# Performance work log

Hardware: AMD Instinct MI355X
Metric: run time of the kernel (lower is better)

The kernel has to match this reference:

```python
import jax, jax.numpy as jnp
import numpy as np

N_HEAD = 16
LN_EPS = 1e-5
NEG = -10000.0


def layer_norm(x, g, b):
    mu = jnp.mean(x, axis=-1, keepdims=True)
    var = jnp.mean((x - mu) ** 2, axis=-1, keepdims=True)
    return (x - mu) * jax.lax.rsqrt(var + LN_EPS) * g + b


def split_heads(t):
    B, S, D = t.shape
    return t.reshape(B, S, N_HEAD, D // N_HEAD).transpose(0, 2, 1, 3)  # [B,H,S,hd]


def merge_heads(t):
    B, H, S, hd = t.shape
    return t.transpose(0, 2, 1, 3).reshape(B, S, H * hd)


def attn_core(q, k, v, causal):
    hd = v.shape[-1]
    w = jnp.einsum('bhqd,bhkd->bhqk', q, k) / jnp.sqrt(jnp.float32(hd)).astype(q.dtype)
    if causal:
        S = w.shape[-1]
        mask = jnp.tril(jnp.ones((S, S), dtype=bool))
        w = jnp.where(mask[None, None], w, jnp.asarray(NEG, w.dtype))
    w = jax.nn.softmax(w, axis=-1)
    return jnp.einsum('bhqk,bhkd->bhqd', w, v)


def setup_inputs() -> dict:
    key = jax.random.key(0)
    ks = jax.random.split(key, 12)
    B, S, D = 4, 1024, 1024
    sd = 0.02
    inp = {
        'x': jax.random.normal(ks[0], (B, S, D), jnp.float32),
        'ctx': jax.random.normal(ks[1], (B, S, D), jnp.float32),
        'c_attn_w': jax.random.normal(ks[2], (D, 3 * D), jnp.float32) * sd,
        'c_attn_b': jnp.zeros((3 * D,), jnp.float32),
        'self_proj_w': jax.random.normal(ks[3], (D, D), jnp.float32) * sd,
        'self_proj_b': jnp.zeros((D,), jnp.float32),
        'q_w': jax.random.normal(ks[4], (D, D), jnp.float32) * sd,
        'q_b': jnp.zeros((D,), jnp.float32),
        'kv_w': jax.random.normal(ks[5], (D, 2 * D), jnp.float32) * sd,
        'kv_b': jnp.zeros((2 * D,), jnp.float32),
        'cross_proj_w': jax.random.normal(ks[6], (D, D), jnp.float32) * sd,
        'cross_proj_b': jnp.zeros((D,), jnp.float32),
        'fc_w': jax.random.normal(ks[7], (D, 4 * D), jnp.float32) * sd,
        'fc_b': jnp.zeros((4 * D,), jnp.float32),
        'mlp_proj_w': jax.random.normal(ks[8], (4 * D, D), jnp.float32) * sd,
        'mlp_proj_b': jnp.zeros((D,), jnp.float32),
        'ln1_g': jnp.ones((D,), jnp.float32), 'ln1_b': jnp.zeros((D,), jnp.float32),
        'ln2_g': jnp.ones((D,), jnp.float32), 'ln2_b': jnp.zeros((D,), jnp.float32),
        'ln3_g': jnp.ones((D,), jnp.float32), 'ln3_b': jnp.zeros((D,), jnp.float32),
    }
    return inp


def reference(x, ctx, c_attn_w, c_attn_b, self_proj_w, self_proj_b,
              q_w, q_b, kv_w, kv_b, cross_proj_w, cross_proj_b,
              fc_w, fc_b, mlp_proj_w, mlp_proj_b,
              ln1_g, ln1_b, ln2_g, ln2_b, ln3_g, ln3_b):
    D = x.shape[-1]
    # --- causal self-attention (post-LN residual) ---
    qkv = x @ c_attn_w + c_attn_b
    q, k, v = jnp.split(qkv, 3, axis=-1)
    a = attn_core(split_heads(q), split_heads(k), split_heads(v), causal=True)
    a = merge_heads(a) @ self_proj_w + self_proj_b
    x = layer_norm(x + a, ln1_g, ln1_b)
    # --- cross-attention ---
    q = x @ q_w + q_b
    kv = ctx @ kv_w + kv_b
    k, v = jnp.split(kv, 2, axis=-1)
    a = attn_core(split_heads(q), split_heads(k), split_heads(v), causal=False)
    a = merge_heads(a) @ cross_proj_w + cross_proj_b
    x = layer_norm(x + a, ln2_g, ln2_b)
    # --- MLP (GPT2 gelu_new == tanh-approx gelu) ---
    h = jax.nn.gelu(x @ fc_w + fc_b, approximate=True)
    m = h @ mlp_proj_w + mlp_proj_b
    x = layer_norm(x + m, ln3_g, ln3_b)
    return x
```

## Files before the change

kernel.cpp:

```cpp
#include <hip/hip_runtime.h>

typedef unsigned short u16;
typedef unsigned int   u32;
typedef short bf16x8 __attribute__((ext_vector_type(8)));
typedef unsigned short u16x8 __attribute__((ext_vector_type(8)));
typedef float f32x4 __attribute__((ext_vector_type(4)));

__device__ __forceinline__ float bf2f(u16 u) {
    u32 x = ((u32)u) << 16;
    return __builtin_bit_cast(float, x);
}
__device__ __forceinline__ u16 f2bf(float f) {
    u32 u = __builtin_bit_cast(u32, f);
    u += 0x7fffu + ((u >> 16) & 1u);
    return (u16)(u >> 16);
}
__device__ __forceinline__ float gelu_f(float x) {
    const float u = 0.7978845608028654f * (x + 0.044715f * x * x * x);
    const float e = __expf(-2.f * fabsf(u));
    const float t = __builtin_copysignf((1.f - e) / (1.f + e), u);
    return 0.5f * x * (1.f + t);
}
__device__ __forceinline__ void glds16(const u16* g, u16* l) {
    __builtin_amdgcn_global_load_lds((const __attribute__((address_space(1))) u32*)g,
                                     (__attribute__((address_space(3))) u32*)l, 16, 0, 0);
}

__global__ void sniff_kernel(const u32* __restrict__ p, int* __restrict__ flag) {
    const int i = threadIdx.x;
    const u32 w = p[i * 8191 + 5];
    const u32 e = (w >> 7) & 0xFF;
    const bool absurd = (e >= 1 && e <= 90) || (e >= 160 && e <= 254);
    const unsigned long long m = __ballot(absurd);
    if (i == 0) *flag = (__popcll(m) >= 8) ? 1 : 0;
}

struct CvtPack {
    const void* src[15];
    u16*        dst[15];
    int         n[15];
};
__global__ __launch_bounds__(256) void cvt_many(CvtPack pp, const int* __restrict__ flag) {
    const int f = *flag;
    const int j = blockIdx.y;
    const void* src = pp.src[j];
    u16* dst = pp.dst[j];
    const int n = pp.n[j];
    const int idx = blockIdx.x * 256 + threadIdx.x;
    const int stride = gridDim.x * 256;
    if (f) {
        const float* s = (const float*)src;
        for (int i = idx; i < n; i += stride) dst[i] = f2bf(s[i]);
    } else {
        const u16* s = (const u16*)src;
        for (int i = idx; i < n; i += stride) dst[i] = s[i];
    }
}

__global__ __launch_bounds__(256) void transpose_cv(const void* __restrict__ src,
                                                    u16* __restrict__ dst,
                                                    int Kd, int Nd,
                                                    const int* __restrict__ flag) {
    const int f = *flag;
    __shared__ u16 t[32][33];
    const int tx = threadIdx.x & 31, ty = threadIdx.x >> 5;
    const int x  = blockIdx.x * 32 + tx;
    const int y0 = blockIdx.y * 32;
#pragma unroll
    for (int j = 0; j < 4; ++j) {
        const long idx = (long)(y0 + ty + j * 8) * Nd + x;
        t[ty + j * 8][tx] = f ? f2bf(((const float*)src)[idx]) : ((const u16*)src)[idx];
    }
    __syncthreads();
    const int xo = blockIdx.y * 32 + tx;
#pragma unroll
    for (int j = 0; j < 4; ++j)
        dst[(long)(blockIdx.x * 32 + ty + j * 8) * Kd + xo] = t[tx][ty + j * 8];
}

__global__ __launch_bounds__(256) void ln_kernel(u16* __restrict__ x,
                                                 const u16* __restrict__ g,
                                                 const u16* __restrict__ bta) {
    const int tid = threadIdx.x;
    u16* p = x + (long)blockIdx.x * 1024;
    float v[4];
    float s = 0.f, s2 = 0.f;
#pragma unroll
    for (int i = 0; i < 4; ++i) {
        v[i] = bf2f(p[tid + i * 256]);
        s += v[i]; s2 += v[i] * v[i];
    }
#pragma unroll
    for (int off = 32; off; off >>= 1) {
        s  += __shfl_xor(s, off, 64);
        s2 += __shfl_xor(s2, off, 64);
    }
    __shared__ float ps[8];
    if ((tid & 63) == 0) { ps[(tid >> 6) * 2] = s; ps[(tid >> 6) * 2 + 1] = s2; }
    __syncthreads();
    s  = ps[0] + ps[2] + ps[4] + ps[6];
    s2 = ps[1] + ps[3] + ps[5] + ps[7];
    const float mu  = s * (1.f / 1024.f);
    const float var = s2 * (1.f / 1024.f) - mu * mu;
    const float rs  = rsqrtf(var + 1e-5f);
#pragma unroll
    for (int i = 0; i < 4; ++i) {
        const int c = tid + i * 256;
        p[c] = f2bf((v[i] - mu) * rs * bf2f(g[c]) + bf2f(bta[c]));
    }
}

__global__ __launch_bounds__(256) void ln_out_kernel(const u16* __restrict__ xin,
                                                     const u16* __restrict__ g,
                                                     const u16* __restrict__ bta,
                                                     void* __restrict__ out,
                                                     const int* __restrict__ flag) {
    const int tid = threadIdx.x;
    const u16* p = xin + (long)blockIdx.x * 1024;
    float v[4];
    float s = 0.f, s2 = 0.f;
#pragma unroll
    for (int i = 0; i < 4; ++i) {
        v[i] = bf2f(p[tid + i * 256]);
        s += v[i]; s2 += v[i] * v[i];
    }
#pragma unroll
    for (int off = 32; off; off >>= 1) {
        s  += __shfl_xor(s, off, 64);
        s2 += __shfl_xor(s2, off, 64);
    }
    __shared__ float ps[8];
    if ((tid & 63) == 0) { ps[(tid >> 6) * 2] = s; ps[(tid >> 6) * 2 + 1] = s2; }
    __syncthreads();
    s  = ps[0] + ps[2] + ps[4] + ps[6];
    s2 = ps[1] + ps[3] + ps[5] + ps[7];
    const float mu  = s * (1.f / 1024.f);
    const float var = s2 * (1.f / 1024.f) - mu * mu;
    const float rs  = rsqrtf(var + 1e-5f);
    const int f = *flag;
    if (f) {
        float* o = (float*)out + (long)blockIdx.x * 1024;
#pragma unroll
        for (int i = 0; i < 4; ++i) {
            const int c = tid + i * 256;
            o[c] = (v[i] - mu) * rs * bf2f(g[c]) + bf2f(bta[c]);
        }
    } else {
        u16* o = (u16*)out + (long)blockIdx.x * 1024;
#pragma unroll
        for (int i = 0; i < 4; ++i) {
            const int c = tid + i * 256;
            o[c] = f2bf((v[i] - mu) * rs * bf2f(g[c]) + bf2f(bta[c]));
        }
    }
}

template <int BM, int BN, int EPI>
__global__ __launch_bounds__(512, (BM + BN) <= 256 ? 4 : 2)
void gemm2(const u16* __restrict__ A, const u16* __restrict__ Bt,
           const u16* __restrict__ bias, const u16* __restrict__ res,
           u16* __restrict__ C, int N, int K) {
    constexpr int WM  = BM / 2, WN = BN / 4;
    constexpr int MT  = WM / 16, NT = WN / 16;
    constexpr int ACH = BM / 8;
    constexpr int NCH = (BM + BN) / 8;
    constexpr int CPW = NCH / 8;
    constexpr int BUF = (BM + BN) * 64;

    const int tid  = threadIdx.x;
    const int wave = tid >> 6, lane = tid & 63;
    const int quad = lane >> 4, l16 = lane & 15;
    const int wm = wave >> 2, wn = wave & 3;

    const int gx  = gridDim.x;
    const int nwg = gx * gridDim.y;
    int lin = blockIdx.y * gx + blockIdx.x;
    lin = (lin & 7) * (nwg >> 3) + (lin >> 3);
    const int bx = lin % gx, by = lin / gx;
    const long m0 = (long)by * BM;
    const int  n0 = bx * BN;

    __shared__ u16 L[2][BUF];

    f32x4 acc[MT][NT];
#pragma unroll
    for (int i = 0; i < MT; ++i)
#pragma unroll
        for (int j = 0; j < NT; ++j) acc[i][j] = (f32x4){0.f, 0.f, 0.f, 0.f};

    const int ro   = lane >> 3;
    const int swzk = ((lane & 7) ^ (ro & 7)) << 3;
    const u16* gsrc[CPW];
    u16*       ldst[CPW];
#pragma unroll
    for (int c = 0; c < CPW; ++c) {
        const int ch = wave + c * 8;
        const u16* base = (ch < ACH) ? A : Bt;
        const long grow = (ch < ACH) ? (m0 + ch * 8 + ro)
                                     : ((long)n0 + (ch - ACH) * 8 + ro);
        gsrc[c] = base + grow * K + swzk;
        ldst[c] = (u16*)&L[0][ch * 512];
    }

    auto stage = [&](int ib, int kt) {
#pragma unroll
        for (int c = 0; c < CPW; ++c)
            glds16(gsrc[c] + kt, ldst[c] + ib * BUF);
    };

    const int nk = K >> 6;
    stage(0, 0);
    for (int i = 0; i < nk; ++i) {
        const int ib = i & 1;
        __syncthreads();
        if (i + 1 < nk) stage(ib ^ 1, (i + 1) << 6);
#pragma unroll
        for (int st = 0; st < 2; ++st) {
            bf16x8 af[MT], bfv[NT];
#pragma unroll
            for (int mt = 0; mt < MT; ++mt) {
                const int rr = wm * WM + mt * 16 + l16;
                af[mt] = *(const bf16x8*)&L[ib][rr * 64 + (((st * 4 + quad) ^ (rr & 7)) << 3)];
            }
#pragma unroll
            for (int nt = 0; nt < NT; ++nt) {
                const int rr = wn * WN + nt * 16 + l16;
                bfv[nt] = *(const bf16x8*)&L[ib][BM * 64 + rr * 64 +
                                                 (((st * 4 + quad) ^ (rr & 7)) << 3)];
            }
            __builtin_amdgcn_s_setprio(1);
#pragma unroll
            for (int mt = 0; mt < MT; ++mt)
#pragma unroll
                for (int nt = 0; nt < NT; ++nt)
                    acc[mt][nt] = __builtin_amdgcn_mfma_f32_16x16x32_bf16(af[mt], bfv[nt],
                                                                          acc[mt][nt], 0, 0, 0);
            __builtin_amdgcn_s_setprio(0);
        }
    }

#pragma unroll
    for (int mt = 0; mt < MT; ++mt)
#pragma unroll
        for (int r = 0; r < 4; ++r) {
            const long row = m0 + wm * WM + mt * 16 + quad * 4 + r;
#pragma unroll
            for (int nt = 0; nt < NT; ++nt) {
                const int col = n0 + wn * WN + nt * 16 + l16;
                float v = acc[mt][nt][r] + bf2f(bias[col]);
                if constexpr (EPI == 1) v += bf2f(res[row * N + col]);
                if constexpr (EPI == 2) v = gelu_f(v);
                C[row * N + col] = f2bf(v);
            }
        }
}

#define KSTR 72
#define MASKV -3.0e4f
template <bool CAUSAL>
__global__ __launch_bounds__(256) void attn_kernel(const u16* __restrict__ Qb,
                                                   const u16* __restrict__ Kb,
                                                   const u16* __restrict__ Vb,
                                                   u16* __restrict__ Ob,
                                                   int qstride, int kvstride, int S) {
    const int tid  = threadIdx.x;
    const int wave = tid >> 6, lane = tid & 63;
    const int quad = lane >> 4, l16 = lane & 15;
    const int h = blockIdx.y, b = blockIdx.z;
    const int qt0 = blockIdx.x * 64;
    const long tokbase = (long)b * S;

    __shared__ u16 K_lds[64 * KSTR];
    __shared__ u16 Vt_lds[64 * KSTR];
    __shared__ u16 P_lds[64 * KSTR];

    const u16* qrow = Qb + (tokbase + qt0 + wave * 16 + l16) * qstride + h * 64;
    bf16x8 qf[2];
    qf[0] = *(const bf16x8*)(qrow + quad * 8);
    qf[1] = *(const bf16x8*)(qrow + 32 + quad * 8);

    f32x4 acc[4];
#pragma unroll
    for (int i = 0; i < 4; ++i) acc[i] = (f32x4){0.f, 0.f, 0.f, 0.f};
    float mrow[4], lrow[4];
#pragma unroll
    for (int r = 0; r < 4; ++r) { mrow[r] = MASKV; lrow[r] = 0.f; }

    const int nkt = CAUSAL ? (blockIdx.x + 1) : (S >> 6);
    for (int kt = 0; kt < nkt; ++kt) {
        __syncthreads();
        {
            int c = tid;
#pragma unroll
            for (int it = 0; it < 2; ++it, c += 256) {
                const int key = c >> 3, dp = (c & 7) * 8;
                const u16* src = Kb + (tokbase + kt * 64 + key) * kvstride + h * 64 + dp;
                *(bf16x8*)(&K_lds[key * KSTR + dp]) = *(const bf16x8*)src;
            }
        }
        {
            const int d = tid & 63, kg = tid >> 6;
            u16x8 v0, v1;
#pragma unroll
            for (int j = 0; j < 8; ++j)
                v0[j] = Vb[(tokbase + kt * 64 + kg * 16 + j) * kvstride + h * 64 + d];
#pragma unroll
            for (int j = 0; j < 8; ++j)
                v1[j] = Vb[(tokbase + kt * 64 + kg * 16 + 8 + j) * kvstride + h * 64 + d];
            *(u16x8*)(&Vt_lds[d * KSTR + kg * 16])     = v0;
            *(u16x8*)(&Vt_lds[d * KSTR + kg * 16 + 8]) = v1;
        }
        __syncthreads();

        float p[4][4];
#pragma unroll
        for (int nt = 0; nt < 4; ++nt) {
            f32x4 s = (f32x4){0.f, 0.f, 0.f, 0.f};
#pragma unroll
            for (int st = 0; st < 2; ++st) {
                bf16x8 kf = *(const bf16x8*)(&K_lds[(nt * 16 + l16) * KSTR + st * 32 + quad * 8]);
                s = __builtin_amdgcn_mfma_f32_16x16x32_bf16(qf[st], kf, s, 0, 0, 0);
            }
#pragma unroll
            for (int r = 0; r < 4; ++r) {
                float sv = s[r] * 0.125f;
                if (CAUSAL) {
                    const int qg  = qt0 + wave * 16 + quad * 4 + r;
                    const int kgi = kt * 64 + nt * 16 + l16;
                    if (kgi > qg) sv = MASKV;
                }
                p[nt][r] = sv;
            }
        }
#pragma unroll
        for (int r = 0; r < 4; ++r) {
            float mx = fmaxf(fmaxf(p[0][r], p[1][r]), fmaxf(p[2][r], p[3][r]));
#pragma unroll
            for (int off = 1; off <= 8; off <<= 1) mx = fmaxf(mx, __shfl_xor(mx, off, 64));
            const float newm  = fmaxf(mrow[r], mx);
            const float alpha = __expf(mrow[r] - newm);
            float rs = 0.f;
#pragma unroll
            for (int nt = 0; nt < 4; ++nt) {
                p[nt][r] = __expf(p[nt][r] - newm);
                rs += p[nt][r];
            }
#pragma unroll
            for (int off = 1; off <= 8; off <<= 1) rs += __shfl_xor(rs, off, 64);
            lrow[r] = lrow[r] * alpha + rs;
            mrow[r] = newm;
#pragma unroll
            for (int dt = 0; dt < 4; ++dt) acc[dt][r] *= alpha;
        }
#pragma unroll
        for (int nt = 0; nt < 4; ++nt)
#pragma unroll
            for (int r = 0; r < 4; ++r)
                P_lds[(wave * 16 + quad * 4 + r) * KSTR + nt * 16 + l16] = f2bf(p[nt][r]);
        __syncthreads();
#pragma unroll
        for (int st = 0; st < 2; ++st) {
            bf16x8 pf = *(const bf16x8*)(&P_lds[(wave * 16 + l16) * KSTR + st * 32 + quad * 8]);
#pragma unroll
            for (int dt = 0; dt < 4; ++dt) {
                bf16x8 vf = *(const bf16x8*)(&Vt_lds[(dt * 16 + l16) * KSTR + st * 32 + quad * 8]);
                acc[dt] = __builtin_amdgcn_mfma_f32_16x16x32_bf16(pf, vf, acc[dt], 0, 0, 0);
            }
        }
    }
#pragma unroll
    for (int r = 0; r < 4; ++r) {
        const float inv = 1.f / lrow[r];
        const long row = tokbase + qt0 + wave * 16 + quad * 4 + r;
#pragma unroll
        for (int dt = 0; dt < 4; ++dt)
            Ob[row * 1024 + h * 64 + dt * 16 + l16] = f2bf(acc[dt][r] * inv);
    }
}

extern "C" void kernel_launch(void* const* d_in, const int* in_sizes, int n_in,
                              void* d_out, int out_size, void* d_ws, size_t ws_size,
                              hipStream_t stream) {
    u16* ws = (u16*)d_ws;
    u16* Wt_attn  = ws + 0;
    u16* Wt_self  = ws + 3145728;
    u16* Wt_q     = ws + 4194304;
    u16* Wt_kv    = ws + 5242880;
    u16* Wt_cross = ws + 7340032;
    u16* Wt_fc    = ws + 8388608;
    u16* Wt_mlp   = ws + 12582912;
    u16* qkv      = ws + 16777216;
    u16* q2       = ws + 16777216;
    u16* kv2      = ws + 20971520;
    u16* x2       = ws + 16777216;
    u16* hbuf     = ws + 20971520;
    u16* abuf     = ws + 29360128;
    u16* x1       = ws + 33554432;
    u16* xb       = ws + 37748736;
    u16* y3       = ws + 37748736;
    u16* ctxb     = ws + 41943040;
    u16* P        = ws + 46137344;
    u16* cab = P;            u16* spb = P + 4096;  u16* qb  = P + 8192;
    u16* kvb = P + 12288;    u16* cpb = P + 16384; u16* fcb = P + 20480;
    u16* mpb = P + 24576;
    u16* l1g = P + 28672;  u16* l1b = P + 32768;
    u16* l2g = P + 36864;  u16* l2b = P + 40960;
    u16* l3g = P + 45056;  u16* l3b = P + 49152;
    int* flag = (int*)(ws + 46137344 + 53248);

    const dim3 tb(256);
    const dim3 tg(512);
    const int NTOK = 4096;

    sniff_kernel<<<1, 64, 0, stream>>>((const u32*)d_in[0], flag);

    CvtPack pp;
    pp.src[0] = d_in[0];  pp.dst[0] = xb;   pp.n[0] = NTOK * 1024;
    pp.src[1] = d_in[1];  pp.dst[1] = ctxb; pp.n[1] = NTOK * 1024;
    pp.src[2] = d_in[3];  pp.dst[2] = cab;  pp.n[2] = 3072;
    pp.src[3] = d_in[5];  pp.dst[3] = spb;  pp.n[3] = 1024;
    pp.src[4] = d_in[7];  pp.dst[4] = qb;   pp.n[4] = 1024;
    pp.src[5] = d_in[9];  pp.dst[5] = kvb;  pp.n[5] = 2048;
    pp.src[6] = d_in[11]; pp.dst[6] = cpb;  pp.n[6] = 1024;
    pp.src[7] = d_in[13]; pp.dst[7] = fcb;  pp.n[7] = 4096;
    pp.src[8] = d_in[15]; pp.dst[8] = mpb;  pp.n[8] = 1024;
    pp.src[9] = d_in[16]; pp.dst[9] = l1g;  pp.n[9] = 1024;
    pp.src[10] = d_in[17]; pp.dst[10] = l1b; pp.n[10] = 1024;
    pp.src[11] = d_in[18]; pp.dst[11] = l2g; pp.n[11] = 1024;
    pp.src[12] = d_in[19]; pp.dst[12] = l2b; pp.n[12] = 1024;
    pp.src[13] = d_in[20]; pp.dst[13] = l3g; pp.n[13] = 1024;
    pp.src[14] = d_in[21]; pp.dst[14] = l3b; pp.n[14] = 1024;
    cvt_many<<<dim3(256, 15), tb, 0, stream>>>(pp, flag);

    transpose_cv<<<dim3(96, 32),  tb, 0, stream>>>(d_in[2],  Wt_attn,  1024, 3072, flag);
    transpose_cv<<<dim3(32, 32),  tb, 0, stream>>>(d_in[4],  Wt_self,  1024, 1024, flag);
    transpose_cv<<<dim3(32, 32),  tb, 0, stream>>>(d_in[6],  Wt_q,     1024, 1024, flag);
    transpose_cv<<<dim3(64, 32),  tb, 0, stream>>>(d_in[8],  Wt_kv,    1024, 2048, flag);
    transpose_cv<<<dim3(32, 32),  tb, 0, stream>>>(d_in[10], Wt_cross, 1024, 1024, flag);
    transpose_cv<<<dim3(128, 32), tb, 0, stream>>>(d_in[12], Wt_fc,    1024, 4096, flag);
    transpose_cv<<<dim3(32, 128), tb, 0, stream>>>(d_in[14], Wt_mlp,   4096, 1024, flag);

    gemm2<256, 256, 0><<<dim3(12, 16), tg, 0, stream>>>(xb, Wt_attn, cab, nullptr, qkv, 3072, 1024);
    attn_kernel<true><<<dim3(16, 16, 4), tb, 0, stream>>>(qkv, qkv + 1024, qkv + 2048, abuf,
                                                          3072, 3072, 1024);
    gemm2<128, 128, 1><<<dim3(8, 32), tg, 0, stream>>>(abuf, Wt_self, spb, xb, x1, 1024, 1024);
    ln_kernel<<<NTOK, tb, 0, stream>>>(x1, l1g, l1b);

    gemm2<128, 128, 0><<<dim3(8, 32), tg, 0, stream>>>(x1,   Wt_q,  qb,  nullptr, q2,  1024, 1024);
    gemm2<128, 256, 0><<<dim3(8, 32), tg, 0, stream>>>(ctxb, Wt_kv, kvb, nullptr, kv2, 2048, 1024);
    attn_kernel<false><<<dim3(16, 16, 4), tb, 0, stream>>>(q2, kv2, kv2 + 1024, abuf,
                                                           1024, 2048, 1024);
    gemm2<128, 128, 1><<<dim3(8, 32), tg, 0, stream>>>(abuf, Wt_cross, cpb, x1, x2, 1024, 1024);
    ln_kernel<<<NTOK, tb, 0, stream>>>(x2, l2g, l2b);

    gemm2<256, 256, 2><<<dim3(16, 16), tg, 0, stream>>>(x2, Wt_fc, fcb, nullptr, hbuf, 4096, 1024);
    gemm2<128, 128, 1><<<dim3(8, 32), tg, 0, stream>>>(hbuf, Wt_mlp, mpb, x2, y3, 1024, 4096);
    ln_out_kernel<<<NTOK, tb, 0, stream>>>(y3, l3g, l3b, d_out, flag);
}
```

Before: 542.1 us.

## Double-buffer attention K/V tiles with paired causal query tiles per block

Replaces the attention kernel with a 512-thread version in which each block handles two 64-query tiles. In the causal case a block pairs tile i with tile QT-1-i so every block does the same amount of work. K tiles are loaded asynchronously into LDS with an XOR-swizzled layout, and V is prefetched into registers for the next tile while the current one is computed. This double-buffers the loads and cuts barriers from three per iteration to one, aiming to hide global load latency and remove causal tail imbalance. It costs more LDS and registers per block, which may lower occupancy.

```diff
diff --git a/kernel.cpp b/kernel.cpp
--- a/kernel.cpp
+++ b/kernel.cpp
@@ -258,23 +258,30 @@
 #define KSTR 72
 #define MASKV -3.0e4f
 template <bool CAUSAL>
-__global__ __launch_bounds__(256) void attn_kernel(const u16* __restrict__ Qb,
-                                                   const u16* __restrict__ Kb,
-                                                   const u16* __restrict__ Vb,
-                                                   u16* __restrict__ Ob,
-                                                   int qstride, int kvstride, int S) {
+__global__ __launch_bounds__(512) void attn2(const u16* __restrict__ Qb,
+                                             const u16* __restrict__ Kb,
+                                             const u16* __restrict__ Vb,
+                                             u16* __restrict__ Ob,
+                                             int qstride, int kvstride, int S) {
     const int tid  = threadIdx.x;
     const int wave = tid >> 6, lane = tid & 63;
     const int quad = lane >> 4, l16 = lane & 15;
     const int h = blockIdx.y, b = blockIdx.z;
-    const int qt0 = blockIdx.x * 64;
     const long tokbase = (long)b * S;
-
-    __shared__ u16 K_lds[64 * KSTR];
-    __shared__ u16 Vt_lds[64 * KSTR];
-    __shared__ u16 P_lds[64 * KSTR];
-
-    const u16* qrow = Qb + (tokbase + qt0 + wave * 16 + l16) * qstride + h * 64;
+    const int QT = S >> 6;
+
+    int qtile;
+    if (CAUSAL) qtile = (wave < 4) ? blockIdx.x : (QT - 1 - blockIdx.x);
+    else        qtile = blockIdx.x * 2 + (wave >> 2);
+    const int qbase = qtile * 64 + (wave & 3) * 16;
+    const int nkt = CAUSAL ? (QT - blockIdx.x) : QT;
+    const int myn = CAUSAL ? (qtile + 1) : QT;
+
+    __shared__ u16 K_lds[2][64 * 64];
+    __shared__ u16 Vt_lds[2][64 * KSTR];
+    __shared__ u16 P_lds[128 * KSTR];
+
+    const u16* qrow = Qb + (tokbase + qbase + l16) * qstride + h * 64;
     bf16x8 qf[2];
     qf[0] = *(const bf16x8*)(qrow + quad * 8);
     qf[1] = *(const bf16x8*)(qrow + 32 + quad * 8);
@@ -286,92 +293,98 @@
 #pragma unroll
     for (int r = 0; r < 4; ++r) { mrow[r] = MASKV; lrow[r] = 0.f; }
 
-    const int nkt = CAUSAL ? (blockIdx.x + 1) : (S >> 6);
+    const int kro = lane >> 3;
+    const int ksw = ((lane & 7) ^ kro) << 3;
+    const u16* Kln = Kb + (tokbase + wave * 8 + kro) * kvstride + h * 64 + ksw;
+    const int vd = tid & 63, vkg = tid >> 6;
+    const u16* Vln = Vb + (tokbase + vkg * 8) * kvstride + h * 64 + vd;
+
+    u16x8 vreg;
+    auto loadV = [&](int kt) {
+#pragma unroll
+        for (int jj = 0; jj < 8; ++jj)
+            vreg[jj] = Vln[((long)kt * 64 + jj) * kvstride];
+    };
+
+    loadV(0);
+    glds16(Kln, &K_lds[0][wave * 512]);
+    *(u16x8*)(&Vt_lds[0][vd * KSTR + vkg * 8]) = vreg;
+    __syncthreads();
+
     for (int kt = 0; kt < nkt; ++kt) {
+        const int cur = kt & 1;
+        const bool haveNext = (kt + 1 < nkt);
+        if (haveNext) {
+            glds16(Kln + (long)(kt + 1) * 64 * kvstride, &K_lds[cur ^ 1][wave * 512]);
+            loadV(kt + 1);
+        }
+        if (kt < myn) {
+            float p[4][4];
+#pragma unroll
+            for (int nt = 0; nt < 4; ++nt) {
+                f32x4 s = (f32x4){0.f, 0.f, 0.f, 0.f};
+#pragma unroll
+                for (int st = 0; st < 2; ++st) {
+                    bf16x8 kf = *(const bf16x8*)(&K_lds[cur][(nt * 16 + l16) * 64 +
+                                                  (((st * 4 + quad) ^ (l16 & 7)) << 3)]);
+                    s = __builtin_amdgcn_mfma_f32_16x16x32_bf16(qf[st], kf, s, 0, 0, 0);
+                }
+#pragma unroll
+                for (int r = 0; r < 4; ++r) {
+                    float sv = s[r] * 0.125f;
+                    if (CAUSAL) {
+                        const int qg  = qbase + quad * 4 + r;
+                        const int kgi = kt * 64 + nt * 16 + l16;
+                        if (kgi > qg) sv = MASKV;
+                    }
+                    p[nt][r] = sv;
+                }
+            }
+#pragma unroll
+            for (int r = 0; r < 4; ++r) {
+                float mx = fmaxf(fmaxf(p[0][r], p[1][r]), fmaxf(p[2][r], p[3][r]));
+#pragma unroll
+                for (int off = 1; off <= 8; off <<= 1) mx = fmaxf(mx, __shfl_xor(mx, off, 64));
+                const float newm  = fmaxf(mrow[r], mx);
+                const float alpha = __expf(mrow[r] - newm);
+                float rs = 0.f;
+#pragma unroll
+                for (int nt = 0; nt < 4; ++nt) {
+                    p[nt][r] = __expf(p[nt][r] - newm);
+                    rs += p[nt][r];
+                }
+#pragma unroll
+                for (int off = 1; off <= 8; off <<= 1) rs += __shfl_xor(rs, off, 64);
+                lrow[r] = lrow[r] * alpha + rs;
+                mrow[r] = newm;
+#pragma unroll
+                for (int dt = 0; dt < 4; ++dt) acc[dt][r] *= alpha;
+            }
+#pragma unroll
+            for (int nt = 0; nt < 4; ++nt)
+#pragma unroll
+                for (int r = 0; r < 4; ++r)
+                    P_lds[(wave * 16 + quad * 4 + r) * KSTR + nt * 16 + l16] = f2bf(p[nt][r]);
+#pragma unroll
+            for (int st = 0; st < 2; ++st) {
+                bf16x8 pf = *(const bf16x8*)(&P_lds[(wave * 16 + l16) * KSTR + st * 32 + quad * 8]);
+#pragma unroll
+                for (int dt = 0; dt < 4; ++dt) {
+                    bf16x8 vf = *(const bf16x8*)(&Vt_lds[cur][(dt * 16 + l16) * KSTR +
+                                                              st * 32 + quad * 8]);
+                    acc[dt] = __builtin_amdgcn_mfma_f32_16x16x32_bf16(pf, vf, acc[dt], 0, 0, 0);
+                }
+            }
+        }
+        if (haveNext)
+            *(u16x8*)(&Vt_lds[cur ^ 1][vd * KSTR + vkg * 8]) = vreg;
         __syncthreads();
-        {
-            int c = tid;
-#pragma unroll
-            for (int it = 0; it < 2; ++it, c += 256) {
-                const int key = c >> 3, dp = (c & 7) * 8;
-                const u16* src = Kb + (tokbase + kt * 64 + key) * kvstride + h * 64 + dp;
-                *(bf16x8*)(&K_lds[key * KSTR + dp]) = *(const bf16x8*)src;
-            }
-        }
-        {
-            const int d = tid & 63, kg = tid >> 6;
-            u16x8 v0, v1;
-#pragma unroll
-            for (int j = 0; j < 8; ++j)
-                v0[j] = Vb[(tokbase + kt * 64 + kg * 16 + j) * kvstride + h * 64 + d];
-#pragma unroll
-            for (int j = 0; j < 8; ++j)
-                v1[j] = Vb[(tokbase + kt * 64 + kg * 16 + 8 + j) * kvstride + h * 64 + d];
-            *(u16x8*)(&Vt_lds[d * KSTR + kg * 16])     = v0;
-            *(u16x8*)(&Vt_lds[d * KSTR + kg * 16 + 8]) = v1;
-        }
-        __syncthreads();
-
-        float p[4][4];
-#pragma unroll
-        for (int nt = 0; nt < 4; ++nt) {
-            f32x4 s = (f32x4){0.f, 0.f, 0.f, 0.f};
-#pragma unroll
-            for (int st = 0; st < 2; ++st) {
-                bf16x8 kf = *(const bf16x8*)(&K_lds[(nt * 16 + l16) * KSTR + st * 32 + quad * 8]);
-                s = __builtin_amdgcn_mfma_f32_16x16x32_bf16(qf[st], kf, s, 0, 0, 0);
-            }
-#pragma unroll
-            for (int r = 0; r < 4; ++r) {
-                float sv = s[r] * 0.125f;
-                if (CAUSAL) {
-                    const int qg  = qt0 + wave * 16 + quad * 4 + r;
-                    const int kgi = kt * 64 + nt * 16 + l16;
-                    if (kgi > qg) sv = MASKV;
-                }
-                p[nt][r] = sv;
-            }
-        }
-#pragma unroll
-        for (int r = 0; r < 4; ++r) {
-            float mx = fmaxf(fmaxf(p[0][r], p[1][r]), fmaxf(p[2][r], p[3][r]));
-#pragma unroll
-            for (int off = 1; off <= 8; off <<= 1) mx = fmaxf(mx, __shfl_xor(mx, off, 64));
-            const float newm  = fmaxf(mrow[r], mx);
-            const float alpha = __expf(mrow[r] - newm);
-            float rs = 0.f;
-#pragma unroll
-            for (int nt = 0; nt < 4; ++nt) {
-                p[nt][r] = __expf(p[nt][r] - newm);
-                rs += p[nt][r];
-            }
-#pragma unroll
-            for (int off = 1; off <= 8; off <<= 1) rs += __shfl_xor(rs, off, 64);
-            lrow[r] = lrow[r] * alpha + rs;
-            mrow[r] = newm;
-#pragma unroll
-            for (int dt = 0; dt < 4; ++dt) acc[dt][r] *= alpha;
-        }
-#pragma unroll
-        for (int nt = 0; nt < 4; ++nt)
-#pragma unroll
-            for (int r = 0; r < 4; ++r)
-                P_lds[(wave * 16 + quad * 4 + r) * KSTR + nt * 16 + l16] = f2bf(p[nt][r]);
-        __syncthreads();
-#pragma unroll
-        for (int st = 0; st < 2; ++st) {
-            bf16x8 pf = *(const bf16x8*)(&P_lds[(wave * 16 + l16) * KSTR + st * 32 + quad * 8]);
-#pragma unroll
-            for (int dt = 0; dt < 4; ++dt) {
-                bf16x8 vf = *(const bf16x8*)(&Vt_lds[(dt * 16 + l16) * KSTR + st * 32 + quad * 8]);
-                acc[dt] = __builtin_amdgcn_mfma_f32_16x16x32_bf16(pf, vf, acc[dt], 0, 0, 0);
-            }
-        }
-    }
+    }
+
 #pragma unroll
     for (int r = 0; r < 4; ++r) {
         const float inv = 1.f / lrow[r];
-        const long row = tokbase + qt0 + wave * 16 + quad * 4 + r;
+        const long row = tokbase + qbase + quad * 4 + r;
 #pragma unroll
         for (int dt = 0; dt < 4; ++dt)
             Ob[row * 1024 + h * 64 + dt * 16 + l16] = f2bf(acc[dt][r] * inv);
@@ -441,15 +454,15 @@
     transpose_cv<<<dim3(32, 128), tb, 0, stream>>>(d_in[14], Wt_mlp,   4096, 1024, flag);
 
     gemm2<256, 256, 0><<<dim3(12, 16), tg, 0, stream>>>(xb, Wt_attn, cab, nullptr, qkv, 3072, 1024);
-    attn_kernel<true><<<dim3(16, 16, 4), tb, 0, stream>>>(qkv, qkv + 1024, qkv + 2048, abuf,
-                                                          3072, 3072, 1024);
+    attn2<true><<<dim3(8, 16, 4), tg, 0, stream>>>(qkv, qkv + 1024, qkv + 2048, abuf,
+                                                   3072, 3072, 1024);
     gemm2<128, 128, 1><<<dim3(8, 32), tg, 0, stream>>>(abuf, Wt_self, spb, xb, x1, 1024, 1024);
     ln_kernel<<<NTOK, tb, 0, stream>>>(x1, l1g, l1b);
 
     gemm2<128, 128, 0><<<dim3(8, 32), tg, 0, stream>>>(x1,   Wt_q,  qb,  nullptr, q2,  1024, 1024);
     gemm2<128, 256, 0><<<dim3(8, 32), tg, 0, stream>>>(ctxb, Wt_kv, kvb, nullptr, kv2, 2048, 1024);
-    attn_kernel<false><<<dim3(16, 16, 4), tb, 0, stream>>>(q2, kv2, kv2 + 1024, abuf,
-                                                           1024, 2048, 1024);
+    attn2<false><<<dim3(8, 16, 4), tg, 0, stream>>>(q2, kv2, kv2 + 1024, abuf,
+                                                    1024, 2048, 1024);
     gemm2<128, 128, 1><<<dim3(8, 32), tg, 0, stream>>>(abuf, Wt_cross, cpb, x1, x2, 1024, 1024);
     ln_kernel<<<NTOK, tb, 0, stream>>>(x2, l2g, l2b);
 
```

Result: faster. 513.2 us (-5.3%).
